# Kernel tuning notes

Measured on AMD Instinct MI355X. Metric: run time of the kernel, lower is better.

The kernel has to match this reference:

```python
import jax, jax.numpy as jnp
import numpy as np

EMBED_DIM = 1024
NUM_HEADS = 16
HEAD_DIM = EMBED_DIM // NUM_HEADS
B, S = 8, 1024


def setup_inputs() -> dict:
    key = jax.random.key(0)
    ks = jax.random.split(key, 8)
    scale = 1.0 / np.sqrt(EMBED_DIM)
    return {
        "q": jax.random.normal(ks[0], (B, S, EMBED_DIM), jnp.float32),
        "v": jax.random.normal(ks[1], (B, S, EMBED_DIM), jnp.float32),
        "Wq": jax.random.normal(ks[2], (EMBED_DIM, EMBED_DIM), jnp.float32) * scale,
        "bq": jnp.zeros((EMBED_DIM,), jnp.float32),
        "Wk": jax.random.normal(ks[3], (EMBED_DIM, EMBED_DIM), jnp.float32) * scale,
        "bk": jnp.zeros((EMBED_DIM,), jnp.float32),
        "Wv": jax.random.normal(ks[4], (EMBED_DIM, EMBED_DIM), jnp.float32) * scale,
        "bv": jnp.zeros((EMBED_DIM,), jnp.float32),
    }


def reference(q, v, Wq, bq, Wk, bk, Wv, bv):
    # call(q, v, k=None): k defaults to v, then compute_multihead_attention(q, v, k)
    # maps (q_arg=q, k_arg=v, v_arg=v) in self-attention.
    qp = q @ Wq + bq                     # [B, S, E]
    kp = v @ Wk + bk                     # [B, S, E]
    vp = v @ Wv + bv                     # [B, S, E]
    # split along feature dim into heads (same math as tf.split+concat on batch)
    qh = qp.reshape(B, S, NUM_HEADS, HEAD_DIM)
    kh = kp.reshape(B, S, NUM_HEADS, HEAD_DIM)
    vh = vp.reshape(B, S, NUM_HEADS, HEAD_DIM)
    # NOTE: original scales by 1/sqrt(embed_dim), not 1/sqrt(head_dim)
    scores = jnp.einsum("bqhd,bkhd->bhqk", qh, kh) / np.sqrt(EMBED_DIM)
    att = jax.nn.softmax(scores, axis=-1)
    out = jnp.einsum("bhqk,bkhd->bqhd", att, vh)  # [B, S, H, Dh]
    return out.reshape(B, S, EMBED_DIM)
```

## Files before the change

### kernel.cpp

```cpp
#include <hip/hip_runtime.h>
#include <cstdint>
#include <cstddef>

#define E 1024
#define S 1024
#define NB 8
#define NH 16
#define DH 64

typedef __bf16 bf16_t;
typedef __bf16 bf16x8 __attribute__((ext_vector_type(8)));
typedef __bf16 bf16x4 __attribute__((ext_vector_type(4)));
typedef __bf16 bf16x2 __attribute__((ext_vector_type(2)));
typedef short s16x4 __attribute__((ext_vector_type(4)));
typedef float f32x4 __attribute__((ext_vector_type(4)));

static __device__ __forceinline__ void gload_lds16(const void* g, void* l) {
  __builtin_amdgcn_global_load_lds((const __attribute__((address_space(1))) void*)g,
                                   (__attribute__((address_space(3))) void*)l, 16, 0, 0);
}

static __device__ __forceinline__ float fast_exp2(float x) {
#if __has_builtin(__builtin_amdgcn_exp2f)
  return __builtin_amdgcn_exp2f(x);
#else
  float r;
  asm("v_exp_f32 %0, %1" : "=v"(r) : "v"(x));
  return r;
#endif
}

__global__ __launch_bounds__(256) void convert_kernel(
    const float* __restrict__ q, const float* __restrict__ v,
    bf16_t* __restrict__ qb, bf16_t* __restrict__ vb) {
  const size_t base = ((size_t)blockIdx.x * 256 + threadIdx.x) * 8;
  const size_t stride = (size_t)2048 * 256 * 8;
#pragma unroll
  for (int h = 0; h < 2; ++h) {
    const float* src = h ? v : q;
    bf16_t* dst = h ? vb : qb;
#pragma unroll
    for (int it = 0; it < 2; ++it) {
      const size_t off = base + (size_t)it * stride;
      float4 a = *(const float4*)(src + off);
      float4 b = *(const float4*)(src + off + 4);
      bf16x8 o = {(bf16_t)a.x, (bf16_t)a.y, (bf16_t)a.z, (bf16_t)a.w,
                  (bf16_t)b.x, (bf16_t)b.y, (bf16_t)b.z, (bf16_t)b.w};
      *(bf16x8*)(dst + off) = o;
    }
  }
}

__global__ __launch_bounds__(256) void wtrans_kernel(
    const float* __restrict__ Wq, const float* __restrict__ Wk,
    const float* __restrict__ Wv, bf16_t* __restrict__ Wqt,
    bf16_t* __restrict__ Wkt, bf16_t* __restrict__ Wvt) {
  const float* W = (blockIdx.z == 0) ? Wq : (blockIdx.z == 1) ? Wk : Wv;
  bf16_t* Wt = (blockIdx.z == 0) ? Wqt : (blockIdx.z == 1) ? Wkt : Wvt;
  __shared__ float tile[64][33];
  const int k0 = blockIdx.x * 64, n0 = blockIdx.y * 32;
  const int t = threadIdx.x;
  {
    const float* src = W + (size_t)(k0 + (t >> 2)) * E + n0 + (t & 3) * 8;
    f32x4 a = *(const f32x4*)src;
    f32x4 b = *(const f32x4*)(src + 4);
    float* drow = &tile[t >> 2][(t & 3) * 8];
#pragma unroll
    for (int j = 0; j < 4; ++j) drow[j] = a[j];
#pragma unroll
    for (int j = 0; j < 4; ++j) drow[4 + j] = b[j];
  }
  __syncthreads();
  bf16x8 o;
#pragma unroll
  for (int j = 0; j < 8; ++j) o[j] = (bf16_t)tile[(t & 7) * 8 + j][t >> 3];
  *(bf16x8*)(Wt + (size_t)(n0 + (t >> 3)) * E + k0 + (t & 7) * 8) = o;
}

__global__ __launch_bounds__(256, 2) void gemm3_kernel(
    const bf16_t* __restrict__ qbf, const bf16_t* __restrict__ vbf,
    const bf16_t* __restrict__ Wqt, const bf16_t* __restrict__ Wkt,
    const bf16_t* __restrict__ Wvt, const float* __restrict__ bq,
    const float* __restrict__ bk, const float* __restrict__ bv,
    bf16_t* __restrict__ qp, bf16_t* __restrict__ kp, bf16_t* __restrict__ vp,
    float qscale) {
  extern __shared__ __align__(16) char smem[];

  const int t = threadIdx.x;
  const int wv = t >> 6, l = t & 63;
  const int lc = l & 15, lg = l >> 4;
  const int wc = wv;

  const int nt = blockIdx.y;
  const int sel = nt >> 2;
  const bf16_t* A = sel ? vbf : qbf;
  const bf16_t* Bt = (sel == 0) ? Wqt : (sel == 1) ? Wkt : Wvt;
  const float* bias = (sel == 0) ? bq : (sel == 1) ? bk : bv;
  bf16_t* C = (sel == 0) ? qp : (sel == 1) ? kp : vp;
  const float scale = (sel == 0) ? qscale : 1.0f;

  const int m0 = blockIdx.x * 128;
  const int n0 = (nt & 3) * 256;

  const int rr = t >> 2;
  const int sgE = ((((t & 3) + ((t >> 3) & 3)) & 3)) << 3;
  const bf16_t* aS0 = A + (size_t)(m0 + rr) * E + sgE;
  const bf16_t* aS1 = A + (size_t)(m0 + 64 + rr) * E + sgE;
  const bf16_t* bS0 = Bt + (size_t)(n0 + rr) * E + sgE;
  const bf16_t* bS1 = Bt + (size_t)(n0 + 64 + rr) * E + sgE;
  const bf16_t* bS2 = Bt + (size_t)(n0 + 128 + rr) * E + sgE;
  const bf16_t* bS3 = Bt + (size_t)(n0 + 192 + rr) * E + sgE;

#define STAGE(tile, buf)                          \
  {                                               \
    const int k0_ = (tile) * 32;                  \
    char* d_ = smem + (buf) * 24576 + wv * 1024;  \
    gload_lds16(aS0 + k0_, d_);                   \
    gload_lds16(aS1 + k0_, d_ + 4096);            \
    gload_lds16(bS0 + k0_, d_ + 8192);            \
    gload_lds16(bS1 + k0_, d_ + 12288);           \
    gload_lds16(bS2 + k0_, d_ + 16384);           \
    gload_lds16(bS3 + k0_, d_ + 20480);           \
  }

  const int cRd = ((lg - (lc >> 1)) & 3) << 4;
  const int aRowB = lc * 64 + cRd;
  const int bRowB = 8192 + (wc * 64 + lc) * 64 + cRd;

  f32x4 acc[8][4] = {};

  STAGE(0, 0);
  STAGE(1, 1);
  asm volatile("s_waitcnt vmcnt(6)" ::: "memory");
  asm volatile("s_barrier" ::: "memory");

  int bufC = 0, bufS = 2;
  for (int tk = 0; tk < 32; ++tk) {
    const char* base = smem + bufC * 24576;
    if (tk + 2 < 32) STAGE(tk + 2, bufS);

    bf16x8 fa[8], fb[4];
#pragma unroll
    for (int ni = 0; ni < 4; ++ni)
      fb[ni] = *(const bf16x8*)(base + bRowB + ni * 1024);
#pragma unroll
    for (int mi = 0; mi < 8; ++mi)
      fa[mi] = *(const bf16x8*)(base + aRowB + mi * 1024);

    __builtin_amdgcn_s_setprio(1);
#pragma unroll
    for (int mi = 0; mi < 8; ++mi)
#pragma unroll
      for (int ni = 0; ni < 4; ++ni)
        acc[mi][ni] = __builtin_amdgcn_mfma_f32_16x16x32_bf16(fa[mi], fb[ni], acc[mi][ni], 0, 0, 0);
    __builtin_amdgcn_s_setprio(0);

    if (tk + 2 < 32) {
      asm volatile("s_waitcnt vmcnt(6)" ::: "memory");
    } else if (tk == 30) {
      asm volatile("s_waitcnt vmcnt(0)" ::: "memory");
    }
    if (tk < 31) asm volatile("s_barrier" ::: "memory");
    bufC = (bufC == 2) ? 0 : bufC + 1;
    bufS = (bufS == 2) ? 0 : bufS + 1;
  }
#undef STAGE

#pragma unroll
  for (int ni = 0; ni < 4; ++ni) {
    const int n = n0 + wc * 64 + ni * 16 + lc;
    const float bv_ = bias[n];
#pragma unroll
    for (int mi = 0; mi < 8; ++mi) {
#pragma unroll
      for (int r = 0; r < 4; ++r) {
        const int m = m0 + mi * 16 + lg * 4 + r;
        C[(size_t)m * E + n] = (bf16_t)((acc[mi][ni][r] + bv_) * scale);
      }
    }
  }
}

__global__ __launch_bounds__(256, 2) void attn_kernel(
    const bf16_t* __restrict__ qp, const bf16_t* __restrict__ kp,
    const bf16_t* __restrict__ vp, float* __restrict__ out) {
  __shared__ __align__(16) unsigned char KsB[2][64 * 128];
  __shared__ bf16_t Vs[2][64][72];
  const int t = threadIdx.x;
  const int w = t >> 6, l = t & 63;
  const int lc = l & 15, lg = l >> 4;

  const int swz = (blockIdx.x & 7) * 64 + (blockIdx.x >> 3);
  const int qblk = swz & 3, bh = swz >> 2;
  const int h = bh & 15, b = bh >> 4;
  const int qbase = qblk * 256 + w * 64;
  const size_t bh_off = (size_t)b * S * E + (size_t)h * DH;

  bf16x8 qf[4][2];
#pragma unroll
  for (int qi = 0; qi < 4; ++qi)
#pragma unroll
    for (int kc = 0; kc < 2; ++kc)
      qf[qi][kc] = *(const bf16x8*)(qp + bh_off + (size_t)(qbase + 16 * qi + lc) * E + kc * 32 + lg * 8);

  f32x4 po[4][4] = {};
  float l_[4] = {0.f, 0.f, 0.f, 0.f};

  const int krow = t >> 2, kc4 = t & 3;
  const int vkv2 = (t & 31) * 2, vd0 = (t >> 5) * 8;
  const bf16_t* kbase = kp + bh_off;
  const bf16_t* vbase = vp + bh_off;
  const int ksw = (krow & 7) << 4;

  bf16x8 ka0, ka1, va0, va1;
  {
    const bf16_t* ks = kbase + (size_t)krow * E + kc4 * 16;
    ka0 = *(const bf16x8*)ks;
    ka1 = *(const bf16x8*)(ks + 8);
    const bf16_t* vs = vbase + (size_t)vkv2 * E + vd0;
    va0 = *(const bf16x8*)vs;
    va1 = *(const bf16x8*)(vs + E);
    *(bf16x8*)&KsB[0][krow * 128 + ((kc4 * 32) ^ ksw)] = ka0;
    *(bf16x8*)&KsB[0][krow * 128 + ((kc4 * 32 + 16) ^ ksw)] = ka1;
#pragma unroll
    for (int j = 0; j < 8; ++j) {
      bf16x2 pr;
      pr[0] = va0[j];
      pr[1] = va1[j];
      *(bf16x2*)&Vs[0][vd0 + j][vkv2] = pr;
    }
  }
  int cur = 0;

  for (int kv0 = 0; kv0 < S; kv0 += 64) {
    __syncthreads();

    const bool more = (kv0 + 64 < S);
    if (more) {
      const bf16_t* ks = kbase + (size_t)(kv0 + 64 + krow) * E + kc4 * 16;
      ka0 = *(const bf16x8*)ks;
      ka1 = *(const bf16x8*)(ks + 8);
      const bf16_t* vs = vbase + (size_t)(kv0 + 64 + vkv2) * E + vd0;
      va0 = *(const bf16x8*)vs;
      va1 = *(const bf16x8*)(vs + E);
    }

    bf16x8 pa2[4][2];
    __builtin_amdgcn_s_setprio(1);
#pragma unroll
    for (int kvb = 0; kvb < 4; ++kvb) {
      const int row = kvb * 16 + lc;
      const int sw = (lc & 7) << 4;
      bf16x8 ak0 = *(const bf16x8*)&KsB[cur][row * 128 + ((lg * 16) ^ sw)];
      bf16x8 ak1 = *(const bf16x8*)&KsB[cur][row * 128 + ((64 + lg * 16) ^ sw)];
      f32x4 sc[4] = {};
#pragma unroll
      for (int qi = 0; qi < 4; ++qi) {
        sc[qi] = __builtin_amdgcn_mfma_f32_16x16x32_bf16(ak0, qf[qi][0], sc[qi], 0, 0, 0);
        sc[qi] = __builtin_amdgcn_mfma_f32_16x16x32_bf16(ak1, qf[qi][1], sc[qi], 0, 0, 0);
      }
#pragma unroll
      for (int qi = 0; qi < 4; ++qi) {
        const float e0 = fast_exp2(sc[qi][0]);
        const float e1 = fast_exp2(sc[qi][1]);
        const float e2 = fast_exp2(sc[qi][2]);
        const float e3 = fast_exp2(sc[qi][3]);
        l_[qi] += (e0 + e1) + (e2 + e3);
        const int hi = (kvb & 1) * 4;
        pa2[qi][kvb >> 1][hi + 0] = (bf16_t)e0;
        pa2[qi][kvb >> 1][hi + 1] = (bf16_t)e1;
        pa2[qi][kvb >> 1][hi + 2] = (bf16_t)e2;
        pa2[qi][kvb >> 1][hi + 3] = (bf16_t)e3;
      }
    }

#pragma unroll
    for (int ki = 0; ki < 2; ++ki) {
      bf16x8 av[4];
#pragma unroll
      for (int ni = 0; ni < 4; ++ni) {
        const bf16x4 vlo = *(const bf16x4*)&Vs[cur][16 * ni + lc][32 * ki + 4 * lg];
        const bf16x4 vhi = *(const bf16x4*)&Vs[cur][16 * ni + lc][32 * ki + 16 + 4 * lg];
        av[ni] = __builtin_shufflevector(vlo, vhi, 0, 1, 2, 3, 4, 5, 6, 7);
      }
#pragma unroll
      for (int qi = 0; qi < 4; ++qi)
#pragma unroll
        for (int ni = 0; ni < 4; ++ni)
          po[qi][ni] = __builtin_amdgcn_mfma_f32_16x16x32_bf16(av[ni], pa2[qi][ki], po[qi][ni], 0, 0, 0);
    }
    __builtin_amdgcn_s_setprio(0);

    if (more) {
      const int nb_ = cur ^ 1;
      *(bf16x8*)&KsB[nb_][krow * 128 + ((kc4 * 32) ^ ksw)] = ka0;
      *(bf16x8*)&KsB[nb_][krow * 128 + ((kc4 * 32 + 16) ^ ksw)] = ka1;
#pragma unroll
      for (int j = 0; j < 8; ++j) {
        bf16x2 pr;
        pr[0] = va0[j];
        pr[1] = va1[j];
        *(bf16x2*)&Vs[nb_][vd0 + j][vkv2] = pr;
      }
      cur = nb_;
    }
  }

#pragma unroll
  for (int qi = 0; qi < 4; ++qi) {
    float lt = l_[qi];
    lt += __shfl_xor(lt, 16, 64);
    lt += __shfl_xor(lt, 32, 64);
    const float inv = 1.0f / lt;
    const int qrow = qbase + 16 * qi + lc;
    float* op = out + (size_t)b * S * E + (size_t)qrow * E + h * DH;
#pragma unroll
    for (int ni = 0; ni < 4; ++ni) {
      f32x4 r = po[qi][ni] * inv;
      *(f32x4*)(op + 16 * ni + lg * 4) = r;
    }
  }
}

extern "C" void kernel_launch(void* const* d_in, const int* in_sizes, int n_in,
                              void* d_out, int out_size, void* d_ws, size_t ws_size,
                              hipStream_t stream) {
  const float* q  = (const float*)d_in[0];
  const float* v  = (const float*)d_in[1];
  const float* Wq = (const float*)d_in[2];
  const float* bq = (const float*)d_in[3];
  const float* Wk = (const float*)d_in[4];
  const float* bk = (const float*)d_in[5];
  const float* Wv = (const float*)d_in[6];
  const float* bv = (const float*)d_in[7];
  float* out = (float*)d_out;

  char* ws = (char*)d_ws;
  const size_t MB = 1024 * 1024;
  bf16_t* Wqt = (bf16_t*)(ws);
  bf16_t* Wkt = (bf16_t*)(ws + 2 * MB);
  bf16_t* Wvt = (bf16_t*)(ws + 4 * MB);
  bf16_t* qp  = (bf16_t*)(ws + 6 * MB);
  bf16_t* kp  = (bf16_t*)(ws + 22 * MB);
  bf16_t* vp  = (bf16_t*)(ws + 38 * MB);

  bf16_t* qbf;
  bf16_t* vbf;
  if (ws_size >= 86 * MB) {
    qbf = (bf16_t*)(ws + 54 * MB);
    vbf = (bf16_t*)(ws + 70 * MB);
  } else {
    qbf = (bf16_t*)d_out;
    vbf = qbf + (size_t)NB * S * E;
  }

  (void)hipFuncSetAttribute((const void*)gemm3_kernel,
                            hipFuncAttributeMaxDynamicSharedMemorySize, 73728);

  convert_kernel<<<dim3(2048), 256, 0, stream>>>(q, v, qbf, vbf);
  wtrans_kernel<<<dim3(16, 32, 3), 256, 0, stream>>>(Wq, Wk, Wv, Wqt, Wkt, Wvt);

  const float qscale = 0.03125f * 1.44269504088896f;
  gemm3_kernel<<<dim3(64, 12), 256, 73728, stream>>>(qbf, vbf, Wqt, Wkt, Wvt,
                                                     bq, bk, bv, qp, kp, vp, qscale);
  attn_kernel<<<dim3(512), 256, 0, stream>>>(qp, kp, vp, out);
}
```

Before: 123.2 us.

## Fuse fp32-to-bf16 activation conversion into projection GEMM A-tile loads

Removes the separate convert kernel and has the QKV projection GEMM stream fp32 activations straight into LDS, converting to bf16 after the LDS reads with an XOR swizzle. This drops a full read and write pass over q and v plus one launch. The cost is that each GEMM block now reads the fp32 A tiles, twice the bytes, and repeats the conversion for each of the 12 column blocks. The pipeline also goes from triple to double buffering with a full vmcnt(0) wait every iteration, so less load latency is hidden.

```diff
diff --git a/kernel.cpp b/kernel.cpp
--- a/kernel.cpp
+++ b/kernel.cpp
@@ -12,7 +12,6 @@
 typedef __bf16 bf16x8 __attribute__((ext_vector_type(8)));
 typedef __bf16 bf16x4 __attribute__((ext_vector_type(4)));
 typedef __bf16 bf16x2 __attribute__((ext_vector_type(2)));
-typedef short s16x4 __attribute__((ext_vector_type(4)));
 typedef float f32x4 __attribute__((ext_vector_type(4)));
 
 static __device__ __forceinline__ void gload_lds16(const void* g, void* l) {
@@ -28,27 +27,6 @@
   asm("v_exp_f32 %0, %1" : "=v"(r) : "v"(x));
   return r;
 #endif
-}
-
-__global__ __launch_bounds__(256) void convert_kernel(
-    const float* __restrict__ q, const float* __restrict__ v,
-    bf16_t* __restrict__ qb, bf16_t* __restrict__ vb) {
-  const size_t base = ((size_t)blockIdx.x * 256 + threadIdx.x) * 8;
-  const size_t stride = (size_t)2048 * 256 * 8;
-#pragma unroll
-  for (int h = 0; h < 2; ++h) {
-    const float* src = h ? v : q;
-    bf16_t* dst = h ? vb : qb;
-#pragma unroll
-    for (int it = 0; it < 2; ++it) {
-      const size_t off = base + (size_t)it * stride;
-      float4 a = *(const float4*)(src + off);
-      float4 b = *(const float4*)(src + off + 4);
-      bf16x8 o = {(bf16_t)a.x, (bf16_t)a.y, (bf16_t)a.z, (bf16_t)a.w,
-                  (bf16_t)b.x, (bf16_t)b.y, (bf16_t)b.z, (bf16_t)b.w};
-      *(bf16x8*)(dst + off) = o;
-    }
-  }
 }
 
 __global__ __launch_bounds__(256) void wtrans_kernel(
@@ -77,8 +55,8 @@
   *(bf16x8*)(Wt + (size_t)(n0 + (t >> 3)) * E + k0 + (t & 7) * 8) = o;
 }
 
-__global__ __launch_bounds__(256, 2) void gemm3_kernel(
-    const bf16_t* __restrict__ qbf, const bf16_t* __restrict__ vbf,
+__global__ __launch_bounds__(256, 2) void gemm3f_kernel(
+    const float* __restrict__ qf32, const float* __restrict__ vf32,
     const bf16_t* __restrict__ Wqt, const bf16_t* __restrict__ Wkt,
     const bf16_t* __restrict__ Wvt, const float* __restrict__ bq,
     const float* __restrict__ bk, const float* __restrict__ bv,
@@ -93,7 +71,7 @@
 
   const int nt = blockIdx.y;
   const int sel = nt >> 2;
-  const bf16_t* A = sel ? vbf : qbf;
+  const float* Af = sel ? vf32 : qf32;
   const bf16_t* Bt = (sel == 0) ? Wqt : (sel == 1) ? Wkt : Wvt;
   const float* bias = (sel == 0) ? bq : (sel == 1) ? bk : bv;
   bf16_t* C = (sel == 0) ? qp : (sel == 1) ? kp : vp;
@@ -102,50 +80,60 @@
   const int m0 = blockIdx.x * 128;
   const int n0 = (nt & 3) * 256;
 
+  const int aRow = t >> 3;
+  const int aG = ((t & 7) ^ ((t >> 3) & 7)) * 4;
+  const float* aS = Af + (size_t)(m0 + aRow) * E + aG;
   const int rr = t >> 2;
   const int sgE = ((((t & 3) + ((t >> 3) & 3)) & 3)) << 3;
-  const bf16_t* aS0 = A + (size_t)(m0 + rr) * E + sgE;
-  const bf16_t* aS1 = A + (size_t)(m0 + 64 + rr) * E + sgE;
   const bf16_t* bS0 = Bt + (size_t)(n0 + rr) * E + sgE;
   const bf16_t* bS1 = Bt + (size_t)(n0 + 64 + rr) * E + sgE;
   const bf16_t* bS2 = Bt + (size_t)(n0 + 128 + rr) * E + sgE;
   const bf16_t* bS3 = Bt + (size_t)(n0 + 192 + rr) * E + sgE;
 
-#define STAGE(tile, buf)                          \
-  {                                               \
-    const int k0_ = (tile) * 32;                  \
-    char* d_ = smem + (buf) * 24576 + wv * 1024;  \
-    gload_lds16(aS0 + k0_, d_);                   \
-    gload_lds16(aS1 + k0_, d_ + 4096);            \
-    gload_lds16(bS0 + k0_, d_ + 8192);            \
-    gload_lds16(bS1 + k0_, d_ + 12288);           \
-    gload_lds16(bS2 + k0_, d_ + 16384);           \
-    gload_lds16(bS3 + k0_, d_ + 20480);           \
-  }
-
+#define STAGE(tile, buf)                                \
+  {                                                     \
+    const int k0_ = (tile) * 32;                        \
+    char* ad_ = smem + (buf) * 32768 + wv * 1024;       \
+    char* bd_ = smem + (buf) * 32768 + 16384 + wv * 1024; \
+    gload_lds16(aS + k0_, ad_);                         \
+    gload_lds16(aS + 32 * E + k0_, ad_ + 4096);         \
+    gload_lds16(aS + 64 * E + k0_, ad_ + 8192);         \
+    gload_lds16(aS + 96 * E + k0_, ad_ + 12288);        \
+    gload_lds16(bS0 + k0_, bd_);                        \
+    gload_lds16(bS1 + k0_, bd_ + 4096);                 \
+    gload_lds16(bS2 + k0_, bd_ + 8192);                 \
+    gload_lds16(bS3 + k0_, bd_ + 12288);                \
+  }
+
+  const int lck = lc & 7;
   const int cRd = ((lg - (lc >> 1)) & 3) << 4;
-  const int aRowB = lc * 64 + cRd;
-  const int bRowB = 8192 + (wc * 64 + lc) * 64 + cRd;
+  const int bRowB = 16384 + (wc * 64 + lc) * 64 + cRd;
+  const int aOff0 = (((lg << 1) | 0) ^ lck) << 4;
+  const int aOff1 = (((lg << 1) | 1) ^ lck) << 4;
 
   f32x4 acc[8][4] = {};
 
   STAGE(0, 0);
-  STAGE(1, 1);
-  asm volatile("s_waitcnt vmcnt(6)" ::: "memory");
+  asm volatile("s_waitcnt vmcnt(0)" ::: "memory");
   asm volatile("s_barrier" ::: "memory");
 
-  int bufC = 0, bufS = 2;
+  int buf = 0;
   for (int tk = 0; tk < 32; ++tk) {
-    const char* base = smem + bufC * 24576;
-    if (tk + 2 < 32) STAGE(tk + 2, bufS);
+    const char* base = smem + buf * 32768;
+    if (tk + 1 < 32) STAGE(tk + 1, buf ^ 1);
 
     bf16x8 fa[8], fb[4];
 #pragma unroll
     for (int ni = 0; ni < 4; ++ni)
       fb[ni] = *(const bf16x8*)(base + bRowB + ni * 1024);
 #pragma unroll
-    for (int mi = 0; mi < 8; ++mi)
-      fa[mi] = *(const bf16x8*)(base + aRowB + mi * 1024);
+    for (int mi = 0; mi < 8; ++mi) {
+      const char* ab = base + (mi * 16 + lc) * 128;
+      f32x4 r0 = *(const f32x4*)(ab + aOff0);
+      f32x4 r1 = *(const f32x4*)(ab + aOff1);
+      fa[mi] = (bf16x8){(bf16_t)r0[0], (bf16_t)r0[1], (bf16_t)r0[2], (bf16_t)r0[3],
+                        (bf16_t)r1[0], (bf16_t)r1[1], (bf16_t)r1[2], (bf16_t)r1[3]};
+    }
 
     __builtin_amdgcn_s_setprio(1);
 #pragma unroll
@@ -155,14 +143,11 @@
         acc[mi][ni] = __builtin_amdgcn_mfma_f32_16x16x32_bf16(fa[mi], fb[ni], acc[mi][ni], 0, 0, 0);
     __builtin_amdgcn_s_setprio(0);
 
-    if (tk + 2 < 32) {
-      asm volatile("s_waitcnt vmcnt(6)" ::: "memory");
-    } else if (tk == 30) {
+    if (tk + 1 < 32) {
       asm volatile("s_waitcnt vmcnt(0)" ::: "memory");
-    }
-    if (tk < 31) asm volatile("s_barrier" ::: "memory");
-    bufC = (bufC == 2) ? 0 : bufC + 1;
-    bufS = (bufS == 2) ? 0 : bufS + 1;
+      asm volatile("s_barrier" ::: "memory");
+    }
+    buf ^= 1;
   }
 #undef STAGE
 
@@ -344,24 +329,13 @@
   bf16_t* kp  = (bf16_t*)(ws + 22 * MB);
   bf16_t* vp  = (bf16_t*)(ws + 38 * MB);
 
-  bf16_t* qbf;
-  bf16_t* vbf;
-  if (ws_size >= 86 * MB) {
-    qbf = (bf16_t*)(ws + 54 * MB);
-    vbf = (bf16_t*)(ws + 70 * MB);
-  } else {
-    qbf = (bf16_t*)d_out;
-    vbf = qbf + (size_t)NB * S * E;
-  }
-
-  (void)hipFuncSetAttribute((const void*)gemm3_kernel,
-                            hipFuncAttributeMaxDynamicSharedMemorySize, 73728);
-
-  convert_kernel<<<dim3(2048), 256, 0, stream>>>(q, v, qbf, vbf);
+  (void)hipFuncSetAttribute((const void*)gemm3f_kernel,
+                            hipFuncAttributeMaxDynamicSharedMemorySize, 65536);
+
   wtrans_kernel<<<dim3(16, 32, 3), 256, 0, stream>>>(Wq, Wk, Wv, Wqt, Wkt, Wvt);
 
   const float qscale = 0.03125f * 1.44269504088896f;
-  gemm3_kernel<<<dim3(64, 12), 256, 73728, stream>>>(qbf, vbf, Wqt, Wkt, Wvt,
-                                                     bq, bk, bv, qp, kp, vp, qscale);
+  gemm3f_kernel<<<dim3(64, 12), 256, 65536, stream>>>(q, v, Wqt, Wkt, Wvt,
+                                                      bq, bk, bv, qp, kp, vp, qscale);
   attn_kernel<<<dim3(512), 256, 0, stream>>>(qp, kp, vp, out);
 }
```

Result: no change. 121.6 us (-1.3%).

## Restructure projection GEMM into 8-wave 256x256 tiles with interleaved ping-pong staging

Applied to the files above, without the earlier changes.

The QKV projection GEMM moves from 4-wave 128x256 tiles with a 3-deep K=32 ring buffer to 8-wave 256x256 tiles with K=64 double buffering. The main loop is split into four sub-phases that interleave LDS fragment reads, global-to-LDS prefetch of the next tile and MFMA bursts, with XOR-swizzled LDS addressing. The goal is more data reuse per block and better overlap of loads with MFMA. In exchange it uses 128KB of LDS per block and more barriers, and the grid shrinks to 384 blocks, which may leave some CUs idle or unevenly loaded.

```diff
diff --git a/kernel.cpp b/kernel.cpp
--- a/kernel.cpp
+++ b/kernel.cpp
@@ -12,7 +12,6 @@
 typedef __bf16 bf16x8 __attribute__((ext_vector_type(8)));
 typedef __bf16 bf16x4 __attribute__((ext_vector_type(4)));
 typedef __bf16 bf16x2 __attribute__((ext_vector_type(2)));
-typedef short s16x4 __attribute__((ext_vector_type(4)));
 typedef float f32x4 __attribute__((ext_vector_type(4)));
 
 static __device__ __forceinline__ void gload_lds16(const void* g, void* l) {
@@ -77,7 +76,7 @@
   *(bf16x8*)(Wt + (size_t)(n0 + (t >> 3)) * E + k0 + (t & 7) * 8) = o;
 }
 
-__global__ __launch_bounds__(256, 2) void gemm3_kernel(
+__global__ __launch_bounds__(512, 2) void gemm8w_kernel(
     const bf16_t* __restrict__ qbf, const bf16_t* __restrict__ vbf,
     const bf16_t* __restrict__ Wqt, const bf16_t* __restrict__ Wkt,
     const bf16_t* __restrict__ Wvt, const float* __restrict__ bq,
@@ -89,7 +88,8 @@
   const int t = threadIdx.x;
   const int wv = t >> 6, l = t & 63;
   const int lc = l & 15, lg = l >> 4;
-  const int wc = wv;
+  const int wr = wv >> 2, wc = wv & 3;
+  const int lck = lc & 7;
 
   const int nt = blockIdx.y;
   const int sel = nt >> 2;
@@ -99,72 +99,100 @@
   bf16_t* C = (sel == 0) ? qp : (sel == 1) ? kp : vp;
   const float scale = (sel == 0) ? qscale : 1.0f;
 
-  const int m0 = blockIdx.x * 128;
+  const int m0 = blockIdx.x * 256;
   const int n0 = (nt & 3) * 256;
 
-  const int rr = t >> 2;
-  const int sgE = ((((t & 3) + ((t >> 3) & 3)) & 3)) << 3;
-  const bf16_t* aS0 = A + (size_t)(m0 + rr) * E + sgE;
-  const bf16_t* aS1 = A + (size_t)(m0 + 64 + rr) * E + sgE;
-  const bf16_t* bS0 = Bt + (size_t)(n0 + rr) * E + sgE;
-  const bf16_t* bS1 = Bt + (size_t)(n0 + 64 + rr) * E + sgE;
-  const bf16_t* bS2 = Bt + (size_t)(n0 + 128 + rr) * E + sgE;
-  const bf16_t* bS3 = Bt + (size_t)(n0 + 192 + rr) * E + sgE;
-
-#define STAGE(tile, buf)                          \
-  {                                               \
-    const int k0_ = (tile) * 32;                  \
-    char* d_ = smem + (buf) * 24576 + wv * 1024;  \
-    gload_lds16(aS0 + k0_, d_);                   \
-    gload_lds16(aS1 + k0_, d_ + 4096);            \
-    gload_lds16(bS0 + k0_, d_ + 8192);            \
-    gload_lds16(bS1 + k0_, d_ + 12288);           \
-    gload_lds16(bS2 + k0_, d_ + 16384);           \
-    gload_lds16(bS3 + k0_, d_ + 20480);           \
-  }
-
-  const int cRd = ((lg - (lc >> 1)) & 3) << 4;
-  const int aRowB = lc * 64 + cRd;
-  const int bRowB = 8192 + (wc * 64 + lc) * 64 + cRd;
+  const int srow = t >> 3;
+  const int sg8 = ((t & 7) ^ (srow & 7)) * 8;
+  const bf16_t* aSrc = A + (size_t)(m0 + srow) * E + sg8;
+  const bf16_t* bSrc = Bt + (size_t)(n0 + srow) * E + sg8;
+
+#define GLA(q, kk, dst) gload_lds16(aSrc + (size_t)(q) * 64 * E + (kk), (dst) + (q) * 8192 + wv * 1024)
+#define GLB(q, kk, dst) gload_lds16(bSrc + (size_t)(q) * 64 * E + (kk), (dst) + (q) * 8192 + wv * 1024)
+#define BAR() asm volatile("s_barrier" ::: "memory")
+
+#define RDA(Ab, fa, mih)                                                      \
+  _Pragma("unroll") for (int mi = 0; mi < 4; ++mi) {                          \
+    const char* rp_ = (Ab) + ((wr * 128 + ((mih) + mi) * 16 + lc) << 7);      \
+    fa[mi][0] = *(const bf16x8*)(rp_ + ((lg ^ lck) << 4));                    \
+    fa[mi][1] = *(const bf16x8*)(rp_ + (((4 + lg) ^ lck) << 4));              \
+  }
+#define RDB(Bb, fb, nih)                                                      \
+  _Pragma("unroll") for (int ni = 0; ni < 2; ++ni) {                          \
+    const char* rp_ = (Bb) + ((wc * 64 + ((nih) + ni) * 16 + lc) << 7);       \
+    fb[ni][0] = *(const bf16x8*)(rp_ + ((lg ^ lck) << 4));                    \
+    fb[ni][1] = *(const bf16x8*)(rp_ + (((4 + lg) ^ lck) << 4));              \
+  }
+#define MM(fa, fb, mo, no)                                                    \
+  __builtin_amdgcn_s_setprio(1);                                              \
+  _Pragma("unroll") for (int mi = 0; mi < 4; ++mi)                            \
+      _Pragma("unroll") for (int ni = 0; ni < 2; ++ni)                        \
+          _Pragma("unroll") for (int ks = 0; ks < 2; ++ks)                    \
+              acc[(mo) + mi][(no) + ni] =                                     \
+                  __builtin_amdgcn_mfma_f32_16x16x32_bf16(                    \
+                      fa[mi][ks], fb[ni][ks], acc[(mo) + mi][(no) + ni],      \
+                      0, 0, 0);                                               \
+  __builtin_amdgcn_s_setprio(0);
 
   f32x4 acc[8][4] = {};
 
-  STAGE(0, 0);
-  STAGE(1, 1);
-  asm volatile("s_waitcnt vmcnt(6)" ::: "memory");
-  asm volatile("s_barrier" ::: "memory");
-
-  int bufC = 0, bufS = 2;
-  for (int tk = 0; tk < 32; ++tk) {
-    const char* base = smem + bufC * 24576;
-    if (tk + 2 < 32) STAGE(tk + 2, bufS);
-
-    bf16x8 fa[8], fb[4];
-#pragma unroll
-    for (int ni = 0; ni < 4; ++ni)
-      fb[ni] = *(const bf16x8*)(base + bRowB + ni * 1024);
-#pragma unroll
-    for (int mi = 0; mi < 8; ++mi)
-      fa[mi] = *(const bf16x8*)(base + aRowB + mi * 1024);
-
-    __builtin_amdgcn_s_setprio(1);
-#pragma unroll
-    for (int mi = 0; mi < 8; ++mi)
-#pragma unroll
-      for (int ni = 0; ni < 4; ++ni)
-        acc[mi][ni] = __builtin_amdgcn_mfma_f32_16x16x32_bf16(fa[mi], fb[ni], acc[mi][ni], 0, 0, 0);
-    __builtin_amdgcn_s_setprio(0);
-
-    if (tk + 2 < 32) {
-      asm volatile("s_waitcnt vmcnt(6)" ::: "memory");
-    } else if (tk == 30) {
-      asm volatile("s_waitcnt vmcnt(0)" ::: "memory");
-    }
-    if (tk < 31) asm volatile("s_barrier" ::: "memory");
-    bufC = (bufC == 2) ? 0 : bufC + 1;
-    bufS = (bufS == 2) ? 0 : bufS + 1;
-  }
-#undef STAGE
+  {
+    char* A0 = smem;
+    char* B0 = smem + 32768;
+    GLA(0, 0, A0); GLA(2, 0, A0);
+    GLB(0, 0, B0); GLB(1, 0, B0); GLB(2, 0, B0); GLB(3, 0, B0);
+    GLA(1, 0, A0); GLA(3, 0, A0);
+  }
+  asm volatile("s_waitcnt vmcnt(2)" ::: "memory");
+  BAR();
+
+  int buf = 0;
+  for (int tk = 0; tk < 16; ++tk) {
+    char* Ab = smem + buf * 65536;
+    char* Bb = Ab + 32768;
+    char* An = smem + (buf ^ 1) * 65536;
+    char* Bn = An + 32768;
+    const int kn = (tk + 1) * 64;
+    const bool st = (tk < 15);
+    bf16x8 fa[4][2], fb[2][2];
+
+    RDA(Ab, fa, 0);
+    RDB(Bb, fb, 0);
+    if (st) { GLA(0, kn, An); GLA(2, kn, An); }
+    BAR();
+    MM(fa, fb, 0, 0);
+    BAR();
+
+    RDB(Bb, fb, 2);
+    if (st) { GLB(0, kn, Bn); GLB(1, kn, Bn); }
+    BAR();
+    MM(fa, fb, 0, 2);
+    if (st) asm volatile("s_waitcnt vmcnt(4)" ::: "memory");
+    else    asm volatile("s_waitcnt vmcnt(0)" ::: "memory");
+    BAR();
+
+    RDA(Ab, fa, 4);
+    if (st) { GLB(2, kn, Bn); GLB(3, kn, Bn); }
+    BAR();
+    MM(fa, fb, 4, 2);
+    BAR();
+
+    RDB(Bb, fb, 0);
+    if (st) { GLA(1, kn, An); GLA(3, kn, An); }
+    BAR();
+    MM(fa, fb, 4, 0);
+    if (st) {
+      asm volatile("s_waitcnt vmcnt(2)" ::: "memory");
+      BAR();
+    }
+    buf ^= 1;
+  }
+#undef MM
+#undef RDB
+#undef RDA
+#undef BAR
+#undef GLB
+#undef GLA
 
 #pragma unroll
   for (int ni = 0; ni < 4; ++ni) {
@@ -174,7 +202,7 @@
     for (int mi = 0; mi < 8; ++mi) {
 #pragma unroll
       for (int r = 0; r < 4; ++r) {
-        const int m = m0 + mi * 16 + lg * 4 + r;
+        const int m = m0 + wr * 128 + mi * 16 + lg * 4 + r;
         C[(size_t)m * E + n] = (bf16_t)((acc[mi][ni][r] + bv_) * scale);
       }
     }
@@ -354,14 +382,14 @@
     vbf = qbf + (size_t)NB * S * E;
   }
 
-  (void)hipFuncSetAttribute((const void*)gemm3_kernel,
-                            hipFuncAttributeMaxDynamicSharedMemorySize, 73728);
+  (void)hipFuncSetAttribute((const void*)gemm8w_kernel,
+                            hipFuncAttributeMaxDynamicSharedMemorySize, 131072);
 
   convert_kernel<<<dim3(2048), 256, 0, stream>>>(q, v, qbf, vbf);
   wtrans_kernel<<<dim3(16, 32, 3), 256, 0, stream>>>(Wq, Wk, Wv, Wqt, Wkt, Wvt);
 
   const float qscale = 0.03125f * 1.44269504088896f;
-  gemm3_kernel<<<dim3(64, 12), 256, 73728, stream>>>(qbf, vbf, Wqt, Wkt, Wvt,
-                                                     bq, bk, bv, qp, kp, vp, qscale);
+  gemm8w_kernel<<<dim3(32, 12), 512, 131072, stream>>>(qbf, vbf, Wqt, Wkt, Wvt,
+                                                       bq, bk, bv, qp, kp, vp, qscale);
   attn_kernel<<<dim3(512), 256, 0, stream>>>(qp, kp, vp, out);
 }
```

Result: slower. 126.5 us (+2.7%).
